# Kernel optimization log

Hardware: AMD Instinct MI355X
Metric: run time of the kernel (lower is better)

The kernel has to match this reference:

```python
import jax, jax.numpy as jnp
import numpy as np
from jax.ops import segment_sum

N_NODES = 100000
N_EDGES = 3200000
IN_DIM = 128
HID = 128
INT_DIM = 512
OUT_DIM = 3


def gcn_conv(x, W, b, src, dst, n):
    # PyG GCNConv (eval): add self-loops, symmetric normalization, aggregate, bias.
    loop = jnp.arange(n, dtype=src.dtype)
    s = jnp.concatenate([src, loop])
    d = jnp.concatenate([dst, loop])
    deg = segment_sum(jnp.ones_like(d, dtype=x.dtype), d, num_segments=n)  # [N]
    dinv = jnp.where(deg > 0, jax.lax.rsqrt(jnp.maximum(deg, 1e-12)), 0.0)
    norm = dinv[s] * dinv[d]                      # [E+N]
    h = x @ W                                      # [N, F_out]
    msg = h[s] * norm[:, None]                    # gather + scale
    return segment_sum(msg, d, num_segments=n) + b


def setup_inputs() -> dict:
    key = jax.random.key(0)
    ks = jax.random.split(key, 12)
    def lin(kw, kb, fi, fo):
        lim = 1.0 / np.sqrt(fi)
        W = jax.random.uniform(kw, (fi, fo), jnp.float32, -lim, lim)
        b = jax.random.uniform(kb, (fo,), jnp.float32, -lim, lim)
        return W, b
    x = jax.random.normal(ks[0], (N_NODES, IN_DIM), jnp.float32)
    edge_index = jax.random.randint(ks[1], (2, N_EDGES), 0, N_NODES, dtype=jnp.int64)
    W1, b1 = lin(ks[2], ks[3], IN_DIM, HID)
    W2, b2 = lin(ks[4], ks[5], HID, HID)
    W3, b3 = lin(ks[6], ks[7], HID, INT_DIM)
    Wi, bi = lin(ks[8], ks[9], INT_DIM, INT_DIM)
    Wc, bc = lin(ks[10], ks[11], INT_DIM, OUT_DIM)
    return {"x": x, "edge_index": edge_index, "W1": W1, "b1": b1, "W2": W2,
            "b2": b2, "W3": W3, "b3": b3, "Wi": Wi, "bi": bi, "Wc": Wc, "bc": bc}


def reference(x, edge_index, W1, b1, W2, b2, W3, b3, Wi, bi, Wc, bc):
    src, dst = edge_index[0], edge_index[1]
    n = x.shape[0]
    h = jax.nn.relu(gcn_conv(x, W1, b1, src, dst, n))
    h = jax.nn.relu(gcn_conv(h, W2, b2, src, dst, n))
    h = jax.nn.relu(gcn_conv(h, W3, b3, src, dst, n))
    h = jax.nn.relu(h @ Wi + bi)
    return h @ Wc + bc
```

## Files before the change

kernel.cpp:

```cpp
#include <hip/hip_runtime.h>
#include <hip/hip_fp16.h>

#define NN 100000
#define NE 3200000
#define NB 391
#define NBLK 512
#define EPB 6250

typedef unsigned int uint32;
typedef unsigned short u16;
typedef long long ll64;
typedef __attribute__((ext_vector_type(8))) _Float16 half8;
typedef __attribute__((ext_vector_type(4))) float f32x4;

__device__ inline float2 h2f2(uint32 u) {
  __half2 h = *reinterpret_cast<__half2*>(&u);
  return __half22float2(h);
}
__device__ inline uint32 f2h2(float x, float y) {
  return (uint32)__half_as_ushort(__float2half(x)) |
         ((uint32)__half_as_ushort(__float2half(y)) << 16);
}
__device__ inline int edge_at(const void* ei, int is64, ll64 idx) {
  return is64 ? (int)((const ll64*)ei)[idx] : ((const int*)ei)[idx];
}

__global__ void k_probe(const int* __restrict__ ei, int* __restrict__ flag) {
  if (threadIdx.x == 0) {
    int acc = 0;
#pragma unroll
    for (int i = 1; i < 32; i += 2) acc |= ei[i];
    *flag = (acc == 0) ? 1 : 0;
  }
}

__global__ __launch_bounds__(256) void k_binB(const void* __restrict__ ei,
                                              const int* __restrict__ flag,
                                              int* __restrict__ tbl) {
  __shared__ int h[NB];
  int k = blockIdx.x, tid = threadIdx.x;
  for (int i = tid; i < NB; i += 256) h[i] = 0;
  __syncthreads();
  int is64 = *flag;
  ll64 beg = (ll64)k * EPB, end = beg + EPB;
  for (ll64 i = beg + tid; i < end; i += 256)
    atomicAdd(&h[edge_at(ei, is64, (ll64)NE + i) >> 8], 1);
  __syncthreads();
  for (int i = tid; i < NB; i += 256) tbl[k * NB + i] = h[i];
}
__global__ __launch_bounds__(512) void k_binC1(int* __restrict__ tbl,
                                               int* __restrict__ total) {
  __shared__ int sd[NBLK];
  int b = blockIdx.x, tid = threadIdx.x;
  int v = tbl[tid * NB + b];
  sd[tid] = v;
  __syncthreads();
  for (int off = 1; off < NBLK; off <<= 1) {
    int t = (tid >= off) ? sd[tid - off] : 0;
    __syncthreads();
    sd[tid] += t;
    __syncthreads();
  }
  tbl[tid * NB + b] = sd[tid] - v;
  if (tid == NBLK - 1) total[b] = sd[NBLK - 1];
}
__global__ __launch_bounds__(512) void k_binC2(const int* __restrict__ total,
                                               int* __restrict__ bbase,
                                               int* __restrict__ offs) {
  __shared__ int sd[512];
  int tid = threadIdx.x;
  int v = (tid < NB) ? total[tid] : 0;
  sd[tid] = v;
  __syncthreads();
  for (int off = 1; off < 512; off <<= 1) {
    int t = (tid >= off) ? sd[tid - off] : 0;
    __syncthreads();
    sd[tid] += t;
    __syncthreads();
  }
  if (tid < NB) bbase[tid] = sd[tid] - v;
  if (tid == 0) offs[NN] = NE;
}
__global__ __launch_bounds__(256) void k_binD(const void* __restrict__ ei,
                                              const int* __restrict__ flag,
                                              const int* __restrict__ tbl,
                                              const int* __restrict__ bbase,
                                              uint32* __restrict__ binned) {
  __shared__ int lb[NB];
  __shared__ int lc[NB];
  int k = blockIdx.x, tid = threadIdx.x;
  for (int i = tid; i < NB; i += 256) {
    lb[i] = tbl[k * NB + i] + bbase[i];
    lc[i] = 0;
  }
  __syncthreads();
  int is64 = *flag;
  ll64 beg = (ll64)k * EPB, end = beg + EPB;
  for (ll64 i = beg + tid; i < end; i += 256) {
    int s = edge_at(ei, is64, i);
    int d = edge_at(ei, is64, (ll64)NE + i);
    int b = d >> 8;
    int r = atomicAdd(&lc[b], 1);
    binned[lb[b] + r] = (uint32)s | ((uint32)(d & 255) << 24);
  }
}
__global__ __launch_bounds__(256) void k_binE(const uint32* __restrict__ binned,
                                              const int* __restrict__ bbase,
                                              const int* __restrict__ total,
                                              int* __restrict__ offs,
                                              float* __restrict__ dinv,
                                              int* __restrict__ csr) {
  __shared__ int cnt[256], pref[256], fil[256];
  int b = blockIdx.x, tid = threadIdx.x;
  cnt[tid] = 0;
  fil[tid] = 0;
  __syncthreads();
  int base = bbase[b], tot = total[b];
  for (int i = tid; i < tot; i += 256) atomicAdd(&cnt[binned[base + i] >> 24], 1);
  __syncthreads();
  int v = cnt[tid];
  pref[tid] = v;
  __syncthreads();
  for (int off = 1; off < 256; off <<= 1) {
    int t = (tid >= off) ? pref[tid - off] : 0;
    __syncthreads();
    pref[tid] += t;
    __syncthreads();
  }
  int myoff = pref[tid] - v;
  pref[tid] = myoff;
  int node = b * 256 + tid;
  if (node < NN) {
    offs[node] = base + myoff;
    dinv[node] = rsqrtf((float)(v + 1));
  }
  __syncthreads();
  for (int i = tid; i < tot; i += 256) {
    uint32 w = binned[base + i];
    int dl = w >> 24;
    int r = atomicAdd(&fil[dl], 1);
    csr[base + pref[dl] + r] = (int)(w & 0xFFFFFFu);
  }
}

__device__ inline void packOne(const float* __restrict__ W, u16* __restrict__ ph,
                               int K, int N, int t) {
  int j = t & 7, lane = (t >> 3) & 63, tl = t >> 9;
  int kbn = K >> 5;
  int kb = tl % kbn, ntile = tl / kbn;
  int k = kb * 32 + (lane >> 4) * 8 + j;
  int n2 = ntile * 16 + (lane & 15);
  ph[t] = __half_as_ushort(__float2half(W[k * N + n2]));
}
__global__ void k_packAll(const float* W1, const float* W2, const float* W3,
                          const float* Wi, u16* p1, u16* p2, u16* p3, u16* pi) {
  int t = blockIdx.x * blockDim.x + threadIdx.x;
  if (t < 16384) packOne(W1, p1, 128, 128, t);
  else if (t < 32768) packOne(W2, p2, 128, 128, t - 16384);
  else if (t < 98304) packOne(W3, p3, 128, 512, t - 32768);
  else if (t < 360448) packOne(Wi, pi, 512, 512, t - 98304);
}

__global__ void k_half(const float4* __restrict__ x, ushort4* __restrict__ xh, int n4) {
  int i = blockIdx.x * blockDim.x + threadIdx.x;
  if (i < n4) {
    float4 v = x[i];
    ushort4 o;
    o.x = __half_as_ushort(__float2half(v.x));
    o.y = __half_as_ushort(__float2half(v.y));
    o.z = __half_as_ushort(__float2half(v.z));
    o.w = __half_as_ushort(__float2half(v.w));
    xh[i] = o;
  }
}

__global__ void k_agg(const uint32* __restrict__ xi, uint32* __restrict__ o,
                      const int* __restrict__ csr, const int* __restrict__ offs,
                      const float* __restrict__ dinv, int n) {
  int node = blockIdx.x * 4 + (threadIdx.x >> 6);
  int lane = threadIdx.x & 63;
  if (node >= n) return;
  int beg = offs[node], end = offs[node + 1];
  float ax = 0.f, ay = 0.f;
  int j = beg;
  for (; j + 3 < end; j += 4) {
    int s0 = csr[j], s1 = csr[j + 1], s2 = csr[j + 2], s3 = csr[j + 3];
    float d0 = dinv[s0], d1 = dinv[s1], d2 = dinv[s2], d3 = dinv[s3];
    float2 r0 = h2f2(xi[(ll64)s0 * 64 + lane]);
    float2 r1 = h2f2(xi[(ll64)s1 * 64 + lane]);
    float2 r2 = h2f2(xi[(ll64)s2 * 64 + lane]);
    float2 r3 = h2f2(xi[(ll64)s3 * 64 + lane]);
    ax += d0 * r0.x + d1 * r1.x + d2 * r2.x + d3 * r3.x;
    ay += d0 * r0.y + d1 * r1.y + d2 * r2.y + d3 * r3.y;
  }
  for (; j < end; j++) {
    int s = csr[j];
    float d = dinv[s];
    float2 r = h2f2(xi[(ll64)s * 64 + lane]);
    ax += d * r.x;
    ay += d * r.y;
  }
  float di = dinv[node];
  float2 sf = h2f2(xi[(ll64)node * 64 + lane]);
  float vx = di * (ax + di * sf.x);
  float vy = di * (ay + di * sf.y);
  o[(ll64)node * 64 + lane] = f2h2(vx, vy);
}

__global__ __launch_bounds__(256, 4) void k_gemm_mfma(
    const u16* __restrict__ A, const u16* __restrict__ Bp,
    const float* __restrict__ bias, u16* __restrict__ Co, int M, int N, int K) {
  int wave = threadIdx.x >> 6, lane = threadIdx.x & 63;
  int quad = lane >> 4, l16 = lane & 15;
  int row0 = blockIdx.x * 64, col0 = blockIdx.y * 64;
  int m = row0 + wave * 16 + l16;
  int mc = (m < M) ? m : (M - 1);
  int kbn = K >> 5;
  f32x4 acc[4] = {{0,0,0,0},{0,0,0,0},{0,0,0,0},{0,0,0,0}};
  const half8* Ar = (const half8*)&A[(ll64)mc * K];
  half8 ac = Ar[quad];
  half8 an = ac;
  half8 bc_[4], bn_[4];
#pragma unroll
  for (int nt = 0; nt < 4; nt++)
    bc_[nt] = *(const half8*)&Bp[((ll64)(((col0 >> 4) + nt) * kbn) * 64 + lane) * 8];
  for (int kb = 0; kb < kbn; kb++) {
    int kn = kb + 1;
    if (kn < kbn) {
      an = Ar[kn * 4 + quad];
#pragma unroll
      for (int nt = 0; nt < 4; nt++)
        bn_[nt] = *(const half8*)&Bp[((ll64)(((col0 >> 4) + nt) * kbn + kn) * 64 + lane) * 8];
    }
#pragma unroll
    for (int nt = 0; nt < 4; nt++)
      acc[nt] = __builtin_amdgcn_mfma_f32_16x16x32_f16(ac, bc_[nt], acc[nt], 0, 0, 0);
    ac = an;
#pragma unroll
    for (int nt = 0; nt < 4; nt++) bc_[nt] = bn_[nt];
  }
#pragma unroll
  for (int nt = 0; nt < 4; nt++) {
    int cc = col0 + nt * 16 + l16;
    float bv = bias[cc];
#pragma unroll
    for (int r = 0; r < 4; r++) {
      int rr = row0 + wave * 16 + quad * 4 + r;
      if (rr < M)
        Co[(ll64)rr * N + cc] =
            __half_as_ushort(__float2half(fmaxf(acc[nt][r] + bv, 0.0f)));
    }
  }
}

__global__ __launch_bounds__(256, 4) void k_tail32(
    const u16* __restrict__ a3, const u16* __restrict__ W3p,
    const float* __restrict__ b3, const u16* __restrict__ Wip,
    const float* __restrict__ bi, const float* __restrict__ Wc,
    const float* __restrict__ bc, float* __restrict__ out, int M) {
  __shared__ u16 h3s[32 * 512];
  __shared__ float sRed[4][32][3];
  int tid = threadIdx.x;
  int wave = tid >> 6, lane = tid & 63, quad = lane >> 4, l16 = lane & 15;
  int row0 = blockIdx.x * 32;

  half8 af[2][4];
#pragma unroll
  for (int rt = 0; rt < 2; rt++) {
    const half8* Ar = (const half8*)&a3[(ll64)(row0 + rt * 16 + l16) * 128];
#pragma unroll
    for (int kb = 0; kb < 4; kb++) af[rt][kb] = Ar[kb * 4 + quad];
  }
  {
    f32x4 acc0 = {0, 0, 0, 0}, acc1 = {0, 0, 0, 0};
    half8 bcur = *(const half8*)&W3p[((ll64)(wave * 32) * 64 + lane) * 8];
    half8 bnxt = bcur;
    for (int t = 0; t < 32; t++) {
      if (t + 1 < 32)
        bnxt = *(const half8*)&W3p[((ll64)(wave * 32 + t + 1) * 64 + lane) * 8];
      int kb = t & 3;
      acc0 = __builtin_amdgcn_mfma_f32_16x16x32_f16(af[0][kb], bcur, acc0, 0, 0, 0);
      acc1 = __builtin_amdgcn_mfma_f32_16x16x32_f16(af[1][kb], bcur, acc1, 0, 0, 0);
      if (kb == 3) {
        int nt = wave * 8 + (t >> 2);
        int col = nt * 16 + l16;
        float bv = b3[col];
#pragma unroll
        for (int r = 0; r < 4; r++) {
          int row0l = quad * 4 + r;
          float v0 = fmaxf(acc0[r] + bv, 0.0f);
          float v1 = fmaxf(acc1[r] + bv, 0.0f);
          int oct0 = (col >> 3) ^ (row0l & 7);
          h3s[row0l * 512 + oct0 * 8 + (col & 7)] = __half_as_ushort(__float2half(v0));
          int row1l = 16 + row0l;
          int oct1 = (col >> 3) ^ (row1l & 7);
          h3s[row1l * 512 + oct1 * 8 + (col & 7)] = __half_as_ushort(__float2half(v1));
        }
        acc0 = (f32x4){0, 0, 0, 0};
        acc1 = (f32x4){0, 0, 0, 0};
      }
      bcur = bnxt;
    }
  }
  __syncthreads();

  float acc3[2][4][3] = {};
  {
    f32x4 acc0 = {0, 0, 0, 0}, acc1 = {0, 0, 0, 0};
    half8 bcur = *(const half8*)&Wip[((ll64)(wave * 128) * 64 + lane) * 8];
    half8 bnxt = bcur;
    int r0l = l16, r1l = 16 + l16;
    int sw0 = r0l & 7;
    for (int t = 0; t < 128; t++) {
      if (t + 1 < 128)
        bnxt = *(const half8*)&Wip[((ll64)(wave * 128 + t + 1) * 64 + lane) * 8];
      int kb = t & 15;
      int oct = ((kb * 4 + quad) ^ sw0);
      half8 a0 = *(const half8*)&h3s[r0l * 512 + oct * 8];
      half8 a1 = *(const half8*)&h3s[r1l * 512 + oct * 8];
      acc0 = __builtin_amdgcn_mfma_f32_16x16x32_f16(a0, bcur, acc0, 0, 0, 0);
      acc1 = __builtin_amdgcn_mfma_f32_16x16x32_f16(a1, bcur, acc1, 0, 0, 0);
      if (kb == 15) {
        int nt = wave * 8 + (t >> 4);
        int col = nt * 16 + l16;
        float bv = bi[col];
        float w0 = Wc[col * 3 + 0], w1 = Wc[col * 3 + 1], w2 = Wc[col * 3 + 2];
#pragma unroll
        for (int r = 0; r < 4; r++) {
          float v0 = fmaxf(acc0[r] + bv, 0.0f);
          float v1 = fmaxf(acc1[r] + bv, 0.0f);
          acc3[0][r][0] += v0 * w0; acc3[0][r][1] += v0 * w1; acc3[0][r][2] += v0 * w2;
          acc3[1][r][0] += v1 * w0; acc3[1][r][1] += v1 * w1; acc3[1][r][2] += v1 * w2;
        }
        acc0 = (f32x4){0, 0, 0, 0};
        acc1 = (f32x4){0, 0, 0, 0};
      }
      bcur = bnxt;
    }
  }
#pragma unroll
  for (int rt = 0; rt < 2; rt++)
#pragma unroll
    for (int r = 0; r < 4; r++)
#pragma unroll
      for (int c = 0; c < 3; c++) {
        float v = acc3[rt][r][c];
        v += __shfl_xor(v, 1);
        v += __shfl_xor(v, 2);
        v += __shfl_xor(v, 4);
        v += __shfl_xor(v, 8);
        acc3[rt][r][c] = v;
      }
  if (l16 == 0) {
#pragma unroll
    for (int rt = 0; rt < 2; rt++)
#pragma unroll
      for (int r = 0; r < 4; r++)
#pragma unroll
        for (int c = 0; c < 3; c++)
          sRed[wave][rt * 16 + quad * 4 + r][c] = acc3[rt][r][c];
  }
  __syncthreads();
  if (tid < 96) {
    int row = tid / 3, c = tid % 3;
    out[(ll64)(row0 + row) * 3 + c] = sRed[0][row][c] + sRed[1][row][c] +
                                      sRed[2][row][c] + sRed[3][row][c] + bc[c];
  }
}

extern "C" void kernel_launch(void* const* d_in, const int* in_sizes, int n_in,
                              void* d_out, int out_size, void* d_ws, size_t ws_size,
                              hipStream_t stream) {
  const float* x  = (const float*)d_in[0];
  const void*  ei = d_in[1];
  const float* W1 = (const float*)d_in[2];
  const float* b1 = (const float*)d_in[3];
  const float* W2 = (const float*)d_in[4];
  const float* b2 = (const float*)d_in[5];
  const float* W3 = (const float*)d_in[6];
  const float* b3 = (const float*)d_in[7];
  const float* Wi = (const float*)d_in[8];
  const float* bi = (const float*)d_in[9];
  const float* Wc = (const float*)d_in[10];
  const float* bc = (const float*)d_in[11];
  float* out = (float*)d_out;

  char* ws = (char*)d_ws;
  const ll64 KB = 1ll << 10, MB = 1ll << 20;
  float* dinv  = (float*)(ws + 0);
  int*   offs  = (int*)(ws + 512 * KB);
  int*   flag  = (int*)(ws + 1 * MB);
  int*   total = (int*)(ws + 1 * MB + 64 * KB);
  int*   bbase = (int*)(ws + 1 * MB + 128 * KB);
  int*   tbl   = (int*)(ws + 1 * MB + 192 * KB);
  uint32* binned = (uint32*)(ws + 2 * MB);
  int*   csr   = (int*)(ws + 15 * MB);
  u16* pW1 = (u16*)(ws + 28 * MB);
  u16* pW2 = (u16*)(ws + 28 * MB + 64 * KB);
  u16* pW3 = (u16*)(ws + 28 * MB + 128 * KB);
  u16* pWi = (u16*)(ws + 28 * MB + 512 * KB);
  u16* xh   = (u16*)(ws + 29 * MB);
  u16* bufA = (u16*)(ws + 55 * MB);
  u16* bufB = (u16*)(ws + 81 * MB);

  const int TB = 256;
  k_probe<<<1, 64, 0, stream>>>((const int*)ei, flag);
  k_binB<<<NBLK, TB, 0, stream>>>(ei, flag, tbl);
  k_binC1<<<NB, NBLK, 0, stream>>>(tbl, total);
  k_binC2<<<1, 512, 0, stream>>>(total, bbase, offs);
  k_binD<<<NBLK, TB, 0, stream>>>(ei, flag, tbl, bbase, binned);
  k_binE<<<NB, TB, 0, stream>>>(binned, bbase, total, offs, dinv, csr);
  k_packAll<<<1408, TB, 0, stream>>>(W1, W2, W3, Wi, pW1, pW2, pW3, pWi);
  k_half<<<(NN * 32 + TB - 1) / TB, TB, 0, stream>>>((const float4*)x,
                                                     (ushort4*)xh, NN * 32);

  const int MBk = (NN + 63) / 64;
  int aggBlocks = (NN + 3) / 4;
  dim3 g128(MBk, 2);

  k_agg<<<aggBlocks, TB, 0, stream>>>((const uint32*)xh, (uint32*)bufA, csr, offs, dinv, NN);
  k_gemm_mfma<<<g128, TB, 0, stream>>>(bufA, pW1, b1, bufB, NN, 128, 128);
  k_agg<<<aggBlocks, TB, 0, stream>>>((const uint32*)bufB, (uint32*)bufA, csr, offs, dinv, NN);
  k_gemm_mfma<<<g128, TB, 0, stream>>>(bufA, pW2, b2, bufB, NN, 128, 128);
  k_agg<<<aggBlocks, TB, 0, stream>>>((const uint32*)bufB, (uint32*)bufA, csr, offs, dinv, NN);
  k_tail32<<<NN / 32, TB, 0, stream>>>(bufA, pW3, b3, pWi, bi, Wc, bc, out, NN);
}
```

Before: 752.1 us.

## Pre-scale features by source dinv to drop per-edge dinv gathers in aggregation

Moves the source-side normalization out of the edge loop. Input features are multiplied by dinv during the fp16 conversion, and each GEMM epilogue multiplies its output rows by dinv, so the aggregation kernel only sums gathered rows and applies the destination dinv once. This removes a random dinv gather per edge, and the gather loop is unrolled to 8 for more loads in flight. The separate probe kernel is folded into the binning kernels, and the pack and half kernels are merged to cut launches. Scaling before the fp16 rounding slightly changes numerics.

Result: faster. 716.0 us (-4.8%).

```diff
diff --git a/kernel.cpp b/kernel.cpp
--- a/kernel.cpp
+++ b/kernel.cpp
@@ -24,24 +24,22 @@
 __device__ inline int edge_at(const void* ei, int is64, ll64 idx) {
   return is64 ? (int)((const ll64*)ei)[idx] : ((const int*)ei)[idx];
 }
-
-__global__ void k_probe(const int* __restrict__ ei, int* __restrict__ flag) {
-  if (threadIdx.x == 0) {
-    int acc = 0;
-#pragma unroll
-    for (int i = 1; i < 32; i += 2) acc |= ei[i];
-    *flag = (acc == 0) ? 1 : 0;
-  }
+__device__ inline int detect64(const int* ei32) {
+  int acc = 0;
+#pragma unroll
+  for (int k = 1; k < 32; k += 2) acc |= ei32[k];
+  return (acc == 0) ? 1 : 0;
 }
 
 __global__ __launch_bounds__(256) void k_binB(const void* __restrict__ ei,
-                                              const int* __restrict__ flag,
                                               int* __restrict__ tbl) {
   __shared__ int h[NB];
+  __shared__ int sIs64;
   int k = blockIdx.x, tid = threadIdx.x;
   for (int i = tid; i < NB; i += 256) h[i] = 0;
-  __syncthreads();
-  int is64 = *flag;
+  if (tid == 0) sIs64 = detect64((const int*)ei);
+  __syncthreads();
+  int is64 = sIs64;
   ll64 beg = (ll64)k * EPB, end = beg + EPB;
   for (ll64 i = beg + tid; i < end; i += 256)
     atomicAdd(&h[edge_at(ei, is64, (ll64)NE + i) >> 8], 1);
@@ -82,19 +80,20 @@
   if (tid == 0) offs[NN] = NE;
 }
 __global__ __launch_bounds__(256) void k_binD(const void* __restrict__ ei,
-                                              const int* __restrict__ flag,
                                               const int* __restrict__ tbl,
                                               const int* __restrict__ bbase,
                                               uint32* __restrict__ binned) {
   __shared__ int lb[NB];
   __shared__ int lc[NB];
+  __shared__ int sIs64;
   int k = blockIdx.x, tid = threadIdx.x;
   for (int i = tid; i < NB; i += 256) {
     lb[i] = tbl[k * NB + i] + bbase[i];
     lc[i] = 0;
   }
-  __syncthreads();
-  int is64 = *flag;
+  if (tid == 0) sIs64 = detect64((const int*)ei);
+  __syncthreads();
+  int is64 = sIs64;
   ll64 beg = (ll64)k * EPB, end = beg + EPB;
   for (ll64 i = beg + tid; i < end; i += 256) {
     int s = edge_at(ei, is64, i);
@@ -152,25 +151,27 @@
   int n2 = ntile * 16 + (lane & 15);
   ph[t] = __half_as_ushort(__float2half(W[k * N + n2]));
 }
-__global__ void k_packAll(const float* W1, const float* W2, const float* W3,
-                          const float* Wi, u16* p1, u16* p2, u16* p3, u16* pi) {
+__global__ void k_packhalf(const float* W1, const float* W2, const float* W3,
+                           const float* Wi, u16* p1, u16* p2, u16* p3, u16* pi,
+                           const float4* __restrict__ x, ushort4* __restrict__ xh,
+                           const float* __restrict__ dinv) {
   int t = blockIdx.x * blockDim.x + threadIdx.x;
   if (t < 16384) packOne(W1, p1, 128, 128, t);
   else if (t < 32768) packOne(W2, p2, 128, 128, t - 16384);
   else if (t < 98304) packOne(W3, p3, 128, 512, t - 32768);
   else if (t < 360448) packOne(Wi, pi, 512, 512, t - 98304);
-}
-
-__global__ void k_half(const float4* __restrict__ x, ushort4* __restrict__ xh, int n4) {
-  int i = blockIdx.x * blockDim.x + threadIdx.x;
-  if (i < n4) {
-    float4 v = x[i];
-    ushort4 o;
-    o.x = __half_as_ushort(__float2half(v.x));
-    o.y = __half_as_ushort(__float2half(v.y));
-    o.z = __half_as_ushort(__float2half(v.z));
-    o.w = __half_as_ushort(__float2half(v.w));
-    xh[i] = o;
+  else {
+    int i = t - 360448;
+    if (i < NN * 32) {
+      float4 v = x[i];
+      float sc = dinv[i >> 5];
+      ushort4 o;
+      o.x = __half_as_ushort(__float2half(v.x * sc));
+      o.y = __half_as_ushort(__float2half(v.y * sc));
+      o.z = __half_as_ushort(__float2half(v.z * sc));
+      o.w = __half_as_ushort(__float2half(v.w * sc));
+      xh[i] = o;
+    }
   }
 }
 
@@ -183,33 +184,35 @@
   int beg = offs[node], end = offs[node + 1];
   float ax = 0.f, ay = 0.f;
   int j = beg;
-  for (; j + 3 < end; j += 4) {
-    int s0 = csr[j], s1 = csr[j + 1], s2 = csr[j + 2], s3 = csr[j + 3];
-    float d0 = dinv[s0], d1 = dinv[s1], d2 = dinv[s2], d3 = dinv[s3];
-    float2 r0 = h2f2(xi[(ll64)s0 * 64 + lane]);
-    float2 r1 = h2f2(xi[(ll64)s1 * 64 + lane]);
-    float2 r2 = h2f2(xi[(ll64)s2 * 64 + lane]);
-    float2 r3 = h2f2(xi[(ll64)s3 * 64 + lane]);
-    ax += d0 * r0.x + d1 * r1.x + d2 * r2.x + d3 * r3.x;
-    ay += d0 * r0.y + d1 * r1.y + d2 * r2.y + d3 * r3.y;
+  for (; j + 7 < end; j += 8) {
+    int s[8];
+    float2 rr[8];
+#pragma unroll
+    for (int q = 0; q < 8; q++) s[q] = csr[j + q];
+#pragma unroll
+    for (int q = 0; q < 8; q++) rr[q] = h2f2(xi[(ll64)s[q] * 64 + lane]);
+#pragma unroll
+    for (int q = 0; q < 8; q++) {
+      ax += rr[q].x;
+      ay += rr[q].y;
+    }
   }
   for (; j < end; j++) {
-    int s = csr[j];
-    float d = dinv[s];
-    float2 r = h2f2(xi[(ll64)s * 64 + lane]);
-    ax += d * r.x;
-    ay += d * r.y;
+    float2 r = h2f2(xi[(ll64)csr[j] * 64 + lane]);
+    ax += r.x;
+    ay += r.y;
   }
   float di = dinv[node];
   float2 sf = h2f2(xi[(ll64)node * 64 + lane]);
-  float vx = di * (ax + di * sf.x);
-  float vy = di * (ay + di * sf.y);
+  float vx = di * (ax + sf.x);
+  float vy = di * (ay + sf.y);
   o[(ll64)node * 64 + lane] = f2h2(vx, vy);
 }
 
 __global__ __launch_bounds__(256, 4) void k_gemm_mfma(
     const u16* __restrict__ A, const u16* __restrict__ Bp,
-    const float* __restrict__ bias, u16* __restrict__ Co, int M, int N, int K) {
+    const float* __restrict__ bias, const float* __restrict__ dscale,
+    u16* __restrict__ Co, int M, int N, int K) {
   int wave = threadIdx.x >> 6, lane = threadIdx.x & 63;
   int quad = lane >> 4, l16 = lane & 15;
   int row0 = blockIdx.x * 64, col0 = blockIdx.y * 64;
@@ -239,6 +242,12 @@
 #pragma unroll
     for (int nt = 0; nt < 4; nt++) bc_[nt] = bn_[nt];
   }
+  float ds[4];
+#pragma unroll
+  for (int r = 0; r < 4; r++) {
+    int rr = row0 + wave * 16 + quad * 4 + r;
+    ds[r] = dscale[(rr < M) ? rr : (M - 1)];
+  }
 #pragma unroll
   for (int nt = 0; nt < 4; nt++) {
     int cc = col0 + nt * 16 + l16;
@@ -248,7 +257,7 @@
       int rr = row0 + wave * 16 + quad * 4 + r;
       if (rr < M)
         Co[(ll64)rr * N + cc] =
-            __half_as_ushort(__float2half(fmaxf(acc[nt][r] + bv, 0.0f)));
+            __half_as_ushort(__float2half(fmaxf(acc[nt][r] + bv, 0.0f) * ds[r]));
     }
   }
 }
@@ -389,7 +398,6 @@
   const ll64 KB = 1ll << 10, MB = 1ll << 20;
   float* dinv  = (float*)(ws + 0);
   int*   offs  = (int*)(ws + 512 * KB);
-  int*   flag  = (int*)(ws + 1 * MB);
   int*   total = (int*)(ws + 1 * MB + 64 * KB);
   int*   bbase = (int*)(ws + 1 * MB + 128 * KB);
   int*   tbl   = (int*)(ws + 1 * MB + 192 * KB);
@@ -404,24 +412,22 @@
   u16* bufB = (u16*)(ws + 81 * MB);
 
   const int TB = 256;
-  k_probe<<<1, 64, 0, stream>>>((const int*)ei, flag);
-  k_binB<<<NBLK, TB, 0, stream>>>(ei, flag, tbl);
+  k_binB<<<NBLK, TB, 0, stream>>>(ei, tbl);
   k_binC1<<<NB, NBLK, 0, stream>>>(tbl, total);
   k_binC2<<<1, 512, 0, stream>>>(total, bbase, offs);
-  k_binD<<<NBLK, TB, 0, stream>>>(ei, flag, tbl, bbase, binned);
+  k_binD<<<NBLK, TB, 0, stream>>>(ei, tbl, bbase, binned);
   k_binE<<<NB, TB, 0, stream>>>(binned, bbase, total, offs, dinv, csr);
-  k_packAll<<<1408, TB, 0, stream>>>(W1, W2, W3, Wi, pW1, pW2, pW3, pWi);
-  k_half<<<(NN * 32 + TB - 1) / TB, TB, 0, stream>>>((const float4*)x,
-                                                     (ushort4*)xh, NN * 32);
+  k_packhalf<<<(360448 + NN * 32 + TB - 1) / TB, TB, 0, stream>>>(
+      W1, W2, W3, Wi, pW1, pW2, pW3, pWi, (const float4*)x, (ushort4*)xh, dinv);
 
   const int MBk = (NN + 63) / 64;
   int aggBlocks = (NN + 3) / 4;
   dim3 g128(MBk, 2);
 
   k_agg<<<aggBlocks, TB, 0, stream>>>((const uint32*)xh, (uint32*)bufA, csr, offs, dinv, NN);
-  k_gemm_mfma<<<g128, TB, 0, stream>>>(bufA, pW1, b1, bufB, NN, 128, 128);
+  k_gemm_mfma<<<g128, TB, 0, stream>>>(bufA, pW1, b1, dinv, bufB, NN, 128, 128);
   k_agg<<<aggBlocks, TB, 0, stream>>>((const uint32*)bufB, (uint32*)bufA, csr, offs, dinv, NN);
-  k_gemm_mfma<<<g128, TB, 0, stream>>>(bufA, pW2, b2, bufB, NN, 128, 128);
+  k_gemm_mfma<<<g128, TB, 0, stream>>>(bufA, pW2, b2, dinv, bufB, NN, 128, 128);
   k_agg<<<aggBlocks, TB, 0, stream>>>((const uint32*)bufB, (uint32*)bufA, csr, offs, dinv, NN);
   k_tail32<<<NN / 32, TB, 0, stream>>>(bufA, pW3, b3, pWi, bi, Wc, bc, out, NN);
 }
```
